# Performance work log

Measured on AMD Instinct MI355X. Metric: run time of the kernel, lower is better.

Reference implementation:

```python
import jax, jax.numpy as jnp
import numpy as np
from jax import lax

B, N, D, H, FF, K = 8192, 20, 128, 8, 512, 3  # batch*time, nodes, d_model, heads, ffn_dim, conv kernel
EPS = 1e-5


def _ln(x, w, b):
    m = jnp.mean(x, axis=-1, keepdims=True)
    v = jnp.mean((x - m) ** 2, axis=-1, keepdims=True)
    return (x - m) * lax.rsqrt(v + EPS) * w + b


def _conv1d(x, w):
    # x: (B,N,D) -> NCH layout (B,D,N); w: (D_out, D_in, K); SAME padding, no bias
    y = lax.conv_general_dilated(x.transpose(0, 2, 1), w, (1,), 'SAME',
                                 dimension_numbers=('NCH', 'OIH', 'NCH'))
    return y.transpose(0, 2, 1)  # back to (B,N,D)


def setup_inputs() -> dict:
    key = jax.random.key(0)
    ks = jax.random.split(key, 12)
    s = 0.05
    return {
        'x': jax.random.normal(ks[0], (B, N, D), jnp.float32),
        # conv1d QKV projection weights (out_ch, in_ch, kernel)
        'wq': jax.random.normal(ks[1], (D, D, K), jnp.float32) * s,
        'wk': jax.random.normal(ks[2], (D, D, K), jnp.float32) * s,
        'wv': jax.random.normal(ks[3], (D, D, K), jnp.float32) * s,
        # LayerNorms after each conv projection
        'lnq_w': jnp.ones((D,), jnp.float32), 'lnq_b': jnp.zeros((D,), jnp.float32),
        'lnk_w': jnp.ones((D,), jnp.float32), 'lnk_b': jnp.zeros((D,), jnp.float32),
        'lnv_w': jnp.ones((D,), jnp.float32), 'lnv_b': jnp.zeros((D,), jnp.float32),
        # relative position bias table (2N-1, H), trunc_normal std=0.02 approximated
        'rel_table': jax.random.normal(ks[4], (2 * N - 1, H), jnp.float32) * 0.02,
        # global spatial bias (H,N,N) and its learned scale alpha
        'gbias': jax.random.normal(ks[5], (H, N, N), jnp.float32) * 0.02,
        'alpha': jnp.array(1.0, jnp.float32),
        # attention output projection (stored as (in,out): y = x @ wo + bo)
        'wo': jax.random.normal(ks[6], (D, D), jnp.float32) * s,
        'bo': jnp.zeros((D,), jnp.float32),
        # FFN
        'w1': jax.random.normal(ks[7], (D, FF), jnp.float32) * s,
        'b1': jnp.zeros((FF,), jnp.float32),
        'w2': jax.random.normal(ks[8], (FF, D), jnp.float32) * s,
        'b2': jnp.zeros((D,), jnp.float32),
        # encoder LayerNorms
        'n1_w': jnp.ones((D,), jnp.float32), 'n1_b': jnp.zeros((D,), jnp.float32),
        'n2_w': jnp.ones((D,), jnp.float32), 'n2_b': jnp.zeros((D,), jnp.float32),
    }


def reference(x, wq, wk, wv, lnq_w, lnq_b, lnk_w, lnk_b, lnv_w, lnv_b,
              rel_table, gbias, alpha, wo, bo, w1, b1, w2, b2,
              n1_w, n1_b, n2_w, n2_b):
    b = x.shape[0]
    dk = D // H
    # conv QKV projections, each followed by LayerNorm + residual add (eval mode: dropout = identity)
    q = x + _ln(_conv1d(x, wq), lnq_w, lnq_b)
    k = x + _ln(_conv1d(x, wk), lnk_w, lnk_b)
    v = x + _ln(_conv1d(x, wv), lnv_w, lnv_b)
    qh = q.reshape(b, N, H, dk)
    kh = k.reshape(b, N, H, dk)
    vh = v.reshape(b, N, H, dk)
    scores = jnp.einsum('bnhd,bmhd->bhnm', qh, kh) * (1.0 / np.sqrt(dk))
    # relative position bias lookup: (N,N) index into (2N-1,H) table -> (H,N,N)
    idx = jnp.arange(N)[:, None] - jnp.arange(N)[None, :] + (N - 1)
    rpb = rel_table[idx].transpose(2, 0, 1)
    scores = scores + rpb[None] + gbias[None] * alpha
    attn = jax.nn.softmax(scores, axis=-1)
    ctx = jnp.einsum('bhnm,bmhd->bnhd', attn, vh).reshape(b, N, D)
    attn_out = ctx @ wo + bo
    # encoder: residual -> norm1 -> FFN -> residual -> norm2 (post-LN style)
    xr = _ln(x + attn_out, n1_w, n1_b)
    ffn = jax.nn.gelu(xr @ w1 + b1, approximate=False) @ w2 + b2
    return _ln(xr + ffn, n2_w, n2_b)
```

## Files before the change

### kernel.cpp

```cpp
#include <hip/hip_runtime.h>
#include <hip/hip_bf16.h>
#include <math.h>

#define NB 8192
#define NN 20
#define DD 128
#define HH 8
#define FFD 512
#define NROWS (NB * NN)

typedef __attribute__((ext_vector_type(8))) short bf16x8;
typedef __attribute__((ext_vector_type(4))) float f32x4;

__device__ __forceinline__ unsigned short f2bf(float f) {
  union { __hip_bfloat16 h; unsigned short u; } cv; cv.h = __float2bfloat16(f); return cv.u;
}
__device__ __forceinline__ float bf2f(unsigned short u) {
  union { unsigned short u; __hip_bfloat16 h; } cv; cv.u = u; return __bfloat162float(cv.h);
}
__device__ __forceinline__ float gelu_t(float v) {
  float t  = v * v;
  float u2 = v * fmaf(0.0713548162f, t, 1.5957691216f);
  float e  = __expf(u2);
  float r  = __builtin_amdgcn_rcpf(e + 1.0f);
  return fmaf(-v, r, v);
}
__device__ __forceinline__ void gload16(const unsigned short* g, unsigned short* lds) {
  __builtin_amdgcn_global_load_lds(
      (const __attribute__((address_space(1))) unsigned int*)g,
      (__attribute__((address_space(3))) unsigned int*)lds, 16, 0, 0);
}

__global__ __launch_bounds__(256) void prep2(
    const float* __restrict__ wq, const float* __restrict__ wk, const float* __restrict__ wv,
    const float* __restrict__ w1, const float* __restrict__ w2, const float* __restrict__ wo,
    const float* __restrict__ rel, const float* __restrict__ gb, const float* __restrict__ alpha,
    unsigned short* __restrict__ WcF, unsigned short* __restrict__ w1F,
    unsigned short* __restrict__ w2F, unsigned short* __restrict__ woF,
    float* __restrict__ biasT)
{
  int bid = blockIdx.x, t = threadIdx.x;
  if (bid < 288) {
    int nt = bid / 12, kc = bid % 12;
    for (int i = t; i < 512; i += 256) {
      int lane = i >> 3, j = i & 7;
      int k = kc * 32 + (lane >> 4) * 8 + j;
      int c = nt * 16 + (lane & 15);
      int kk = k >> 7, din = k & 127;
      int which = c >> 7, dout = c & 127;
      const float* w = (which == 0) ? wq : (which == 1) ? wk : wv;
      WcF[((nt * 12 + kc) * 64 + lane) * 8 + j] = f2bf(w[(dout * 128 + din) * 3 + kk]);
    }
  } else if (bid < 416) {
    int tt = bid - 288; int nt = tt / 4, kc = tt % 4;
    for (int i = t; i < 512; i += 256) {
      int lane = i >> 3, j = i & 7;
      int k = kc * 32 + (lane >> 4) * 8 + j;
      int c = nt * 16 + (lane & 15);
      w1F[((nt * 4 + kc) * 64 + lane) * 8 + j] = f2bf(w1[k * 512 + c]);
    }
  } else if (bid < 544) {
    int tt = bid - 416; int nt = tt / 16, kc = tt % 16;
    for (int i = t; i < 512; i += 256) {
      int lane = i >> 3, j = i & 7;
      int k = kc * 32 + (lane >> 4) * 8 + j;
      int c = nt * 16 + (lane & 15);
      w2F[((nt * 16 + kc) * 64 + lane) * 8 + j] = f2bf(w2[k * 128 + c]);
    }
  } else if (bid < 576) {
    int tt = bid - 544; int nt = tt / 4, kc = tt % 4;
    for (int i = t; i < 512; i += 256) {
      int lane = i >> 3, j = i & 7;
      int k = kc * 32 + (lane >> 4) * 8 + j;
      int c = nt * 16 + (lane & 15);
      woF[((nt * 4 + kc) * 64 + lane) * 8 + j] = f2bf(wo[k * 128 + c]);
    }
  } else {
    int h = bid - 576; float a = alpha[0];
    for (int i = t; i < 400; i += 256) {
      int n = i / 20, m = i % 20;
      biasT[h * 400 + i] = rel[(n - m + 19) * 8 + h] + gb[h * 400 + i] * a;
    }
  }
}

__global__ __launch_bounds__(256, 3) void conv_qkv(
    const float* __restrict__ x, const unsigned short* __restrict__ WcF,
    const float* __restrict__ lnq_w, const float* __restrict__ lnq_b,
    const float* __restrict__ lnk_w, const float* __restrict__ lnk_b,
    const float* __restrict__ lnv_w, const float* __restrict__ lnv_b,
    unsigned short* __restrict__ qP, unsigned short* __restrict__ kP,
    unsigned short* __restrict__ vP)
{
  __shared__ __align__(16) unsigned short xA[130 * 136];
  __shared__ __align__(16) unsigned short Bb[2][4096];
  unsigned short* Obuf = &Bb[0][0];

  const int t = threadIdx.x;
  const int w = t >> 6, l = t & 63;
  const int l15 = l & 15, l4 = l >> 4;
  const long g0 = (long)blockIdx.x * 128;
  const int chunkA = w * 2, chunkB = w * 2 + 1;

  gload16(WcF + (size_t)(chunkA * 12) * 512 + l * 8, &Bb[0][chunkA * 512]);
  gload16(WcF + (size_t)(chunkB * 12) * 512 + l * 8, &Bb[0][chunkB * 512]);

  for (int i = t; i < 130 * 32; i += 256) {
    int r = i >> 5, c4 = i & 31;
    long g = g0 - 1 + r;
    long gc = g < 0 ? 0 : (g >= NROWS ? NROWS - 1 : g);
    float4 v = *(const float4*)(x + gc * 128 + c4 * 4);
    ushort4 pk; pk.x = f2bf(v.x); pk.y = f2bf(v.y); pk.z = f2bf(v.z); pk.w = f2bf(v.w);
    *(ushort4*)&xA[r * 136 + c4 * 4] = pk;
  }
  __syncthreads();

  const int rA0 = w * 32 + l15;
  const int rA1 = rA0 + 16;
  const int nA0 = (int)((g0 + rA0) % 20);
  const int nA1 = (int)((g0 + rA1) % 20);
  bool mk0[3], mk1[3];
  mk0[0] = (nA0 != 0);  mk0[1] = true; mk0[2] = (nA0 != 19);
  mk1[0] = (nA1 != 0);  mk1[1] = true; mk1[2] = (nA1 != 19);

  const bf16x8 zz = {};
  for (int p = 0; p < 3; ++p) {
    const size_t Wpo = (size_t)p * 8 * 12 * 512;

    f32x4 acc[2][8];
    #pragma unroll
    for (int mt = 0; mt < 2; ++mt)
      #pragma unroll
      for (int nt = 0; nt < 8; ++nt) acc[mt][nt] = (f32x4){0.f, 0.f, 0.f, 0.f};

    for (int kc = 0; kc < 12; ++kc) {
      if (kc < 11) {
        int nb = (kc + 1) & 1;
        gload16(WcF + Wpo + (size_t)(chunkA * 12 + kc + 1) * 512 + l * 8, &Bb[nb][chunkA * 512]);
        gload16(WcF + Wpo + (size_t)(chunkB * 12 + kc + 1) * 512 + l * 8, &Bb[nb][chunkB * 512]);
      }
      const int kk = kc >> 2, k4 = kc & 3;
      bf16x8 a0 = *(const bf16x8*)&xA[(rA0 + kk) * 136 + k4 * 32 + l4 * 8]; if (!mk0[kk]) a0 = zz;
      bf16x8 a1 = *(const bf16x8*)&xA[(rA1 + kk) * 136 + k4 * 32 + l4 * 8]; if (!mk1[kk]) a1 = zz;
      const unsigned short* bb = &Bb[kc & 1][l * 8];
      #pragma unroll
      for (int nt = 0; nt < 8; ++nt) {
        bf16x8 b = *(const bf16x8*)(bb + nt * 512);
        acc[0][nt] = __builtin_amdgcn_mfma_f32_16x16x32_bf16(a0, b, acc[0][nt], 0, 0, 0);
        acc[1][nt] = __builtin_amdgcn_mfma_f32_16x16x32_bf16(a1, b, acc[1][nt], 0, 0, 0);
      }
      __syncthreads();
    }

    const float* lw = (p == 0) ? lnq_w : (p == 1) ? lnk_w : lnv_w;
    const float* lb = (p == 0) ? lnq_b : (p == 1) ? lnk_b : lnv_b;
    const float qs = (p == 0) ? 0.25f : 1.0f;
    unsigned short* plane = (p == 0) ? qP : (p == 1) ? kP : vP;
    float gw8[8], gb8[8];
    #pragma unroll
    for (int nt = 0; nt < 8; ++nt) { gw8[nt] = lw[nt * 16 + l15]; gb8[nt] = lb[nt * 16 + l15]; }

    float meanv[2][4], invv[2][4];
    #pragma unroll
    for (int mt = 0; mt < 2; ++mt) {
      float s[4], qq[4];
      #pragma unroll
      for (int j = 0; j < 4; ++j) {
        float a0 = 0.f, a1 = 0.f;
        #pragma unroll
        for (int nt = 0; nt < 8; ++nt) { float v = acc[mt][nt][j]; a0 += v; a1 = fmaf(v, v, a1); }
        s[j] = a0; qq[j] = a1;
      }
      #pragma unroll
      for (int off = 1; off < 16; off <<= 1) {
        #pragma unroll
        for (int j = 0; j < 4; ++j) { s[j] += __shfl_xor(s[j], off); qq[j] += __shfl_xor(qq[j], off); }
      }
      #pragma unroll
      for (int j = 0; j < 4; ++j) {
        float mean = s[j] * (1.f / 128.f);
        float var  = qq[j] * (1.f / 128.f) - mean * mean;
        meanv[mt][j] = mean;
        invv[mt][j]  = rsqrtf(var + 1e-5f);
      }
    }

    #pragma unroll
    for (int q = 0; q < 2; ++q) {
      #pragma unroll
      for (int mt = 0; mt < 2; ++mt)
        #pragma unroll
        for (int j = 0; j < 4; ++j) {
          int lr = w * 32 + mt * 16 + l4 * 4 + j;
          #pragma unroll
          for (int ntl = 0; ntl < 4; ++ntl) {
            int nt = q * 4 + ntl;
            Obuf[lr * 64 + ntl * 16 + l15] =
                f2bf((acc[mt][nt][j] - meanv[mt][j]) * invv[mt][j] * gw8[nt] + gb8[nt]);
          }
        }
      __syncthreads();
      #pragma unroll
      for (int it = 0; it < 4; ++it) {
        int i = t + it * 256;
        int r = i >> 3, c8 = i & 7;
        bf16x8 ob = *(const bf16x8*)&Obuf[r * 64 + c8 * 8];
        bf16x8 xr8 = *(const bf16x8*)&xA[(r + 1) * 136 + q * 64 + c8 * 8];
        bf16x8 o;
        #pragma unroll
        for (int j = 0; j < 8; ++j)
          o[j] = (short)f2bf((bf2f((unsigned short)xr8[j]) + bf2f((unsigned short)ob[j])) * qs);
        *(bf16x8*)&plane[(g0 + r) * 128 + q * 64 + c8 * 8] = o;
      }
      __syncthreads();
    }

    if (p < 2) {
      size_t Wn = (size_t)(p + 1) * 8 * 12 * 512;
      gload16(WcF + Wn + (size_t)(chunkA * 12) * 512 + l * 8, &Bb[0][chunkA * 512]);
      gload16(WcF + Wn + (size_t)(chunkB * 12) * 512 + l * 8, &Bb[0][chunkB * 512]);
      __syncthreads();
    }
  }
}

__global__ __launch_bounds__(256, 3) void attn_wo(
    const float* __restrict__ x,
    const unsigned short* __restrict__ qP, const unsigned short* __restrict__ kP,
    const unsigned short* __restrict__ vP,
    const unsigned short* __restrict__ woF, const float* __restrict__ biasT,
    const float* __restrict__ bo,
    const float* __restrict__ n1w, const float* __restrict__ n1b,
    unsigned short* __restrict__ xr)
{
  __shared__ __align__(16) char smem[43520];
  unsigned short* ks  = (unsigned short*)smem;
  unsigned short* vs  = (unsigned short*)(smem + 21760);
  unsigned short* ctx = ks;
  unsigned short* scr = vs;

  const int t = threadIdx.x;
  const int w = t >> 6, l = t & 63;
  const int l15 = l & 15, l4 = l >> 4;
  const int eb = blockIdx.x * 4;

  for (int i = t; i < 2560; i += 256) {
    int proj = i / 1280, r = i % 1280;
    int e = r / 320, rr = r % 320;
    int n = rr / 16, c8 = rr % 16;
    const unsigned short* src = (proj == 0 ? kP : vP) + (((size_t)(eb + e) * 20 + n) * 128 + c8 * 8);
    unsigned short* dst = (proj == 0 ? ks : vs) + ((e * 20 + n) * 136 + c8 * 8);
    *(bf16x8*)dst = *(const bf16x8*)src;
  }
  __syncthreads();

  float pm[3][20];
  #pragma unroll
  for (int pass = 0; pass < 3; ++pass) {
    int i = t + pass * 256;
    if (i < 640) {
      int e = i / 160, hh = (i / 20) % 8, n = i % 20;
      const unsigned short* qr = qP + ((size_t)(eb + e) * 20 + n) * 128 + hh * 16;
      bf16x8 qa = *(const bf16x8*)qr, qb = *(const bf16x8*)(qr + 8);
      float q[16];
      #pragma unroll
      for (int j = 0; j < 8; ++j) { q[j] = bf2f((unsigned short)qa[j]); q[8 + j] = bf2f((unsigned short)qb[j]); }
      float bias[20];
      const float* bp = &biasT[(hh * 20 + n) * 20];
      #pragma unroll
      for (int m4 = 0; m4 < 5; ++m4) {
        float4 bv = *(const float4*)(bp + m4 * 4);
        bias[m4 * 4] = bv.x; bias[m4 * 4 + 1] = bv.y; bias[m4 * 4 + 2] = bv.z; bias[m4 * 4 + 3] = bv.w;
      }
      float mx = -1e30f;
      #pragma unroll
      for (int m = 0; m < 20; ++m) {
        const unsigned short* kr = &ks[(e * 20 + m) * 136 + hh * 16];
        bf16x8 ka = *(const bf16x8*)kr, kb = *(const bf16x8*)(kr + 8);
        float sv = bias[m];
        #pragma unroll
        for (int j = 0; j < 8; ++j) {
          sv = fmaf(q[j], bf2f((unsigned short)ka[j]), sv);
          sv = fmaf(q[8 + j], bf2f((unsigned short)kb[j]), sv);
        }
        pm[pass][m] = sv; mx = fmaxf(mx, sv);
      }
      float sum = 0.f;
      #pragma unroll
      for (int m = 0; m < 20; ++m) { pm[pass][m] = __expf(pm[pass][m] - mx); sum += pm[pass][m]; }
      float rs = 1.f / sum;
      #pragma unroll
      for (int m = 0; m < 20; ++m) pm[pass][m] *= rs;
    }
  }
  __syncthreads();

  #pragma unroll
  for (int pass = 0; pass < 3; ++pass) {
    int i = t + pass * 256;
    if (i < 640) {
      int e = i / 160, hh = (i / 20) % 8, n = i % 20;
      float c[16];
      #pragma unroll
      for (int j = 0; j < 16; ++j) c[j] = 0.f;
      #pragma unroll
      for (int m = 0; m < 20; ++m) {
        const unsigned short* vr = &vs[(e * 20 + m) * 136 + hh * 16];
        bf16x8 va = *(const bf16x8*)vr, vb = *(const bf16x8*)(vr + 8);
        float pv = pm[pass][m];
        #pragma unroll
        for (int j = 0; j < 8; ++j) {
          c[j] = fmaf(pv, bf2f((unsigned short)va[j]), c[j]);
          c[8 + j] = fmaf(pv, bf2f((unsigned short)vb[j]), c[8 + j]);
        }
      }
      bf16x8 c0, c1;
      #pragma unroll
      for (int j = 0; j < 8; ++j) { c0[j] = (short)f2bf(c[j]); c1[j] = (short)f2bf(c[8 + j]); }
      *(bf16x8*)&ctx[(e * 20 + n) * 136 + hh * 16] = c0;
      *(bf16x8*)&ctx[(e * 20 + n) * 136 + hh * 16 + 8] = c1;
    }
  }
  __syncthreads();

  {
    f32x4 acc[5][2];
    #pragma unroll
    for (int mt = 0; mt < 5; ++mt)
      #pragma unroll
      for (int i = 0; i < 2; ++i) acc[mt][i] = (f32x4){0.f, 0.f, 0.f, 0.f};
    #pragma unroll
    for (int kc = 0; kc < 4; ++kc) {
      bf16x8 a[5], b[2];
      #pragma unroll
      for (int mt = 0; mt < 5; ++mt) {
        int g = mt * 16 + l15;
        int e = g / 20, n = g % 20;
        a[mt] = *(const bf16x8*)&ctx[(e * 20 + n) * 136 + kc * 32 + l4 * 8];
      }
      #pragma unroll
      for (int i = 0; i < 2; ++i) {
        int ntg = w * 2 + i;
        b[i] = *(const bf16x8*)&woF[((ntg * 4 + kc) * 64 + l) * 8];
      }
      #pragma unroll
      for (int mt = 0; mt < 5; ++mt)
        #pragma unroll
        for (int i = 0; i < 2; ++i)
          acc[mt][i] = __builtin_amdgcn_mfma_f32_16x16x32_bf16(a[mt], b[i], acc[mt][i], 0, 0, 0);
    }
    #pragma unroll
    for (int mt = 0; mt < 5; ++mt)
      #pragma unroll
      for (int i = 0; i < 2; ++i) {
        int col = (w * 2 + i) * 16 + l15;
        int gbase = mt * 16 + l4 * 4;
        #pragma unroll
        for (int j = 0; j < 4; ++j)
          scr[(gbase + j) * 136 + col] = f2bf(acc[mt][i][j]);
      }
  }
  __syncthreads();

  for (int r = w; r < 80; r += 4) {
    int e = r / 20, n = r % 20;
    const float* xrow = x + ((size_t)(eb + e) * 20 + n) * 128;
    float v0 = bf2f(scr[r * 136 + l])      + bo[l]      + xrow[l];
    float v1 = bf2f(scr[r * 136 + 64 + l]) + bo[64 + l] + xrow[64 + l];
    float s = v0 + v1, sq = v0 * v0 + v1 * v1;
    #pragma unroll
    for (int off = 32; off > 0; off >>= 1) { s += __shfl_xor(s, off); sq += __shfl_xor(sq, off); }
    float mean = s * (1.f / 128.f);
    float var  = sq * (1.f / 128.f) - mean * mean;
    float inv  = rsqrtf(var + 1e-5f);
    size_t ro = ((size_t)(eb + e) * 20 + n) * 128;
    xr[ro + l]      = f2bf((v0 - mean) * inv * n1w[l] + n1b[l]);
    xr[ro + 64 + l] = f2bf((v1 - mean) * inv * n1w[64 + l] + n1b[64 + l]);
  }
}

__global__ __launch_bounds__(256, 4) void ffn_c(
    const unsigned short* __restrict__ xr,
    const unsigned short* __restrict__ w1F, const unsigned short* __restrict__ w2F,
    const float* __restrict__ b1, const float* __restrict__ b2,
    const float* __restrict__ n2w, const float* __restrict__ n2b,
    float* __restrict__ out)
{
  __shared__ __align__(16) unsigned short smem[2 * 64 * 136];
  unsigned short* xrb = smem;
  unsigned short* hq  = smem + 64 * 136;
  unsigned short* scr = hq;

  const int t = threadIdx.x;
  const int w = t >> 6, l = t & 63;
  const int l15 = l & 15, l4 = l >> 4;
  const size_t row0 = (size_t)blockIdx.x * 64;

  for (int i = t; i < 1024; i += 256) {
    int r = i >> 4, c8 = i & 15;
    *(bf16x8*)&xrb[r * 136 + c8 * 8] = *(const bf16x8*)&xr[(row0 + r) * 128 + c8 * 8];
  }
  __syncthreads();

  f32x4 acc2[4][2];
  #pragma unroll
  for (int mt = 0; mt < 4; ++mt)
    #pragma unroll
    for (int i = 0; i < 2; ++i) acc2[mt][i] = (f32x4){0.f, 0.f, 0.f, 0.f};

  #pragma unroll
  for (int ph = 0; ph < 4; ++ph) {
    f32x4 acc1[4][2];
    #pragma unroll
    for (int mt = 0; mt < 4; ++mt)
      #pragma unroll
      for (int i = 0; i < 2; ++i) acc1[mt][i] = (f32x4){0.f, 0.f, 0.f, 0.f};
    #pragma unroll
    for (int kc = 0; kc < 4; ++kc) {
      bf16x8 a[4];
      #pragma unroll
      for (int mt = 0; mt < 4; ++mt)
        a[mt] = *(const bf16x8*)&xrb[(mt * 16 + l15) * 136 + kc * 32 + l4 * 8];
      #pragma unroll
      for (int i = 0; i < 2; ++i) {
        int ntg = ph * 8 + w * 2 + i;
        bf16x8 b = *(const bf16x8*)&w1F[((ntg * 4 + kc) * 64 + l) * 8];
        #pragma unroll
        for (int mt = 0; mt < 4; ++mt)
          acc1[mt][i] = __builtin_amdgcn_mfma_f32_16x16x32_bf16(a[mt], b, acc1[mt][i], 0, 0, 0);
      }
    }
    #pragma unroll
    for (int i = 0; i < 2; ++i) {
      int lc = (w * 2 + i) * 16 + l15;
      float b1v = b1[(ph * 8 + w * 2 + i) * 16 + l15];
      #pragma unroll
      for (int mt = 0; mt < 4; ++mt)
        #pragma unroll
        for (int j = 0; j < 4; ++j) {
          float v = acc1[mt][i][j] + b1v;
          hq[(mt * 16 + l4 * 4 + j) * 136 + lc] = f2bf(gelu_t(v));
        }
    }
    __syncthreads();

    #pragma unroll
    for (int kk = 0; kk < 4; ++kk) {
      bf16x8 a[4];
      #pragma unroll
      for (int mt = 0; mt < 4; ++mt)
        a[mt] = *(const bf16x8*)&hq[(mt * 16 + l15) * 136 + kk * 32 + l4 * 8];
      #pragma unroll
      for (int i = 0; i < 2; ++i) {
        int ntg = w * 2 + i;
        int kcg = ph * 4 + kk;
        bf16x8 b = *(const bf16x8*)&w2F[((ntg * 16 + kcg) * 64 + l) * 8];
        #pragma unroll
        for (int mt = 0; mt < 4; ++mt)
          acc2[mt][i] = __builtin_amdgcn_mfma_f32_16x16x32_bf16(a[mt], b, acc2[mt][i], 0, 0, 0);
      }
    }
    __syncthreads();
  }

  #pragma unroll
  for (int mt = 0; mt < 4; ++mt)
    #pragma unroll
    for (int i = 0; i < 2; ++i) {
      int col = (w * 2 + i) * 16 + l15;
      int rbase = mt * 16 + l4 * 4;
      #pragma unroll
      for (int j = 0; j < 4; ++j)
        scr[(rbase + j) * 136 + col] = f2bf(acc2[mt][i][j]);
    }
  __syncthreads();

  for (int r = w; r < 64; r += 4) {
    float v0 = bf2f(scr[r * 136 + l])      + b2[l]      + bf2f(xrb[r * 136 + l]);
    float v1 = bf2f(scr[r * 136 + 64 + l]) + b2[64 + l] + bf2f(xrb[r * 136 + 64 + l]);
    float s = v0 + v1, sq = v0 * v0 + v1 * v1;
    #pragma unroll
    for (int off = 32; off > 0; off >>= 1) { s += __shfl_xor(s, off); sq += __shfl_xor(sq, off); }
    float mean = s * (1.f / 128.f);
    float var  = sq * (1.f / 128.f) - mean * mean;
    float inv  = rsqrtf(var + 1e-5f);
    out[(row0 + r) * 128 + l]      = (v0 - mean) * inv * n2w[l] + n2b[l];
    out[(row0 + r) * 128 + 64 + l] = (v1 - mean) * inv * n2w[64 + l] + n2b[64 + l];
  }
}

extern "C" void kernel_launch(void* const* d_in, const int* in_sizes, int n_in,
                              void* d_out, int out_size, void* d_ws, size_t ws_size,
                              hipStream_t stream) {
  const float* x     = (const float*)d_in[0];
  const float* wq    = (const float*)d_in[1];
  const float* wk    = (const float*)d_in[2];
  const float* wv    = (const float*)d_in[3];
  const float* lnq_w = (const float*)d_in[4];
  const float* lnq_b = (const float*)d_in[5];
  const float* lnk_w = (const float*)d_in[6];
  const float* lnk_b = (const float*)d_in[7];
  const float* lnv_w = (const float*)d_in[8];
  const float* lnv_b = (const float*)d_in[9];
  const float* rel   = (const float*)d_in[10];
  const float* gb    = (const float*)d_in[11];
  const float* alpha = (const float*)d_in[12];
  const float* wo    = (const float*)d_in[13];
  const float* bo    = (const float*)d_in[14];
  const float* w1    = (const float*)d_in[15];
  const float* b1    = (const float*)d_in[16];
  const float* w2    = (const float*)d_in[17];
  const float* b2    = (const float*)d_in[18];
  const float* n1w   = (const float*)d_in[19];
  const float* n1b   = (const float*)d_in[20];
  const float* n2w   = (const float*)d_in[21];
  const float* n2b   = (const float*)d_in[22];
  float* out = (float*)d_out;

  unsigned short* WcF = (unsigned short*)d_ws;
  unsigned short* w1F = WcF + 147456;
  unsigned short* w2F = w1F + 65536;
  unsigned short* woF = w2F + 65536;
  float* biasT = (float*)(woF + 16384);
  unsigned short* xr = (unsigned short*)((char*)d_ws + 602624);

  const size_t NEED2 = 602624ULL + 41943040ULL;

  hipLaunchKernelGGL(prep2, dim3(584), dim3(256), 0, stream,
                     wq, wk, wv, w1, w2, wo, rel, gb, alpha, WcF, w1F, w2F, woF, biasT);

  unsigned short* qP = (unsigned short*)((char*)d_ws + NEED2);
  unsigned short* kP = (unsigned short*)d_out;
  unsigned short* vP = kP + (size_t)NROWS * 128;

  hipLaunchKernelGGL(conv_qkv, dim3(NROWS / 128), dim3(256), 0, stream,
                     x, WcF, lnq_w, lnq_b, lnk_w, lnk_b, lnv_w, lnv_b, qP, kP, vP);
  hipLaunchKernelGGL(attn_wo, dim3(NB / 4), dim3(256), 0, stream,
                     x, qP, kP, vP, woF, biasT, bo, n1w, n1b, xr);
  hipLaunchKernelGGL(ffn_c, dim3(NROWS / 64), dim3(256), 0, stream,
                     xr, w1F, w2F, b1, b2, n2w, n2b, out);
}
```

Before: 276.6 us.

## Swizzle attention LDS layout to drop padding and raise occupancy to four blocks

Replaces the 136-element padded LDS row stride in attn_wo with an unpadded 128 stride plus an XOR swizzle for the ctx and scratch tiles. This shrinks shared memory from 43520 to 40960 bytes and raises the launch bound from 3 to 4 blocks per CU. The QK dot product is also split into four independent accumulators to shorten the FMA dependency chain. K and V reads are left unswizzled at stride 128, which risks LDS bank conflicts, and the tighter register budget may cause spills.

```diff
diff --git a/kernel.cpp b/kernel.cpp
--- a/kernel.cpp
+++ b/kernel.cpp
@@ -29,6 +29,9 @@
   __builtin_amdgcn_global_load_lds(
       (const __attribute__((address_space(1))) unsigned int*)g,
       (__attribute__((address_space(3))) unsigned int*)lds, 16, 0, 0);
+}
+__device__ __forceinline__ int swz80(int row, int col) {
+  return row * 128 + ((((col >> 3) ^ (row & 15)) << 3) | (col & 7));
 }
 
 __global__ __launch_bounds__(256) void prep2(
@@ -224,7 +227,7 @@
   }
 }
 
-__global__ __launch_bounds__(256, 3) void attn_wo(
+__global__ __launch_bounds__(256, 4) void attn_wo(
     const float* __restrict__ x,
     const unsigned short* __restrict__ qP, const unsigned short* __restrict__ kP,
     const unsigned short* __restrict__ vP,
@@ -233,9 +236,9 @@
     const float* __restrict__ n1w, const float* __restrict__ n1b,
     unsigned short* __restrict__ xr)
 {
-  __shared__ __align__(16) char smem[43520];
+  __shared__ __align__(16) char smem[40960];
   unsigned short* ks  = (unsigned short*)smem;
-  unsigned short* vs  = (unsigned short*)(smem + 21760);
+  unsigned short* vs  = (unsigned short*)(smem + 20480);
   unsigned short* ctx = ks;
   unsigned short* scr = vs;
 
@@ -249,7 +252,7 @@
     int e = r / 320, rr = r % 320;
     int n = rr / 16, c8 = rr % 16;
     const unsigned short* src = (proj == 0 ? kP : vP) + (((size_t)(eb + e) * 20 + n) * 128 + c8 * 8);
-    unsigned short* dst = (proj == 0 ? ks : vs) + ((e * 20 + n) * 136 + c8 * 8);
+    unsigned short* dst = (proj == 0 ? ks : vs) + ((e * 20 + n) * 128 + c8 * 8);
     *(bf16x8*)dst = *(const bf16x8*)src;
   }
   __syncthreads();
@@ -275,14 +278,17 @@
       float mx = -1e30f;
       #pragma unroll
       for (int m = 0; m < 20; ++m) {
-        const unsigned short* kr = &ks[(e * 20 + m) * 136 + hh * 16];
+        const unsigned short* kr = &ks[(e * 20 + m) * 128 + hh * 16];
         bf16x8 ka = *(const bf16x8*)kr, kb = *(const bf16x8*)(kr + 8);
-        float sv = bias[m];
-        #pragma unroll
-        for (int j = 0; j < 8; ++j) {
-          sv = fmaf(q[j], bf2f((unsigned short)ka[j]), sv);
-          sv = fmaf(q[8 + j], bf2f((unsigned short)kb[j]), sv);
+        float s0 = bias[m], s1 = 0.f, s2 = 0.f, s3 = 0.f;
+        #pragma unroll
+        for (int j = 0; j < 4; ++j) {
+          s0 = fmaf(q[j],      bf2f((unsigned short)ka[j]),     s0);
+          s1 = fmaf(q[j + 4],  bf2f((unsigned short)ka[j + 4]), s1);
+          s2 = fmaf(q[j + 8],  bf2f((unsigned short)kb[j]),     s2);
+          s3 = fmaf(q[j + 12], bf2f((unsigned short)kb[j + 4]), s3);
         }
+        float sv = (s0 + s1) + (s2 + s3);
         pm[pass][m] = sv; mx = fmaxf(mx, sv);
       }
       float sum = 0.f;
@@ -305,7 +311,7 @@
       for (int j = 0; j < 16; ++j) c[j] = 0.f;
       #pragma unroll
       for (int m = 0; m < 20; ++m) {
-        const unsigned short* vr = &vs[(e * 20 + m) * 136 + hh * 16];
+        const unsigned short* vr = &vs[(e * 20 + m) * 128 + hh * 16];
         bf16x8 va = *(const bf16x8*)vr, vb = *(const bf16x8*)(vr + 8);
         float pv = pm[pass][m];
         #pragma unroll
@@ -317,8 +323,9 @@
       bf16x8 c0, c1;
       #pragma unroll
       for (int j = 0; j < 8; ++j) { c0[j] = (short)f2bf(c[j]); c1[j] = (short)f2bf(c[8 + j]); }
-      *(bf16x8*)&ctx[(e * 20 + n) * 136 + hh * 16] = c0;
-      *(bf16x8*)&ctx[(e * 20 + n) * 136 + hh * 16 + 8] = c1;
+      int re = e * 20 + n;
+      *(bf16x8*)&ctx[swz80(re, hh * 16)]     = c0;
+      *(bf16x8*)&ctx[swz80(re, hh * 16 + 8)] = c1;
     }
   }
   __syncthreads();
@@ -333,11 +340,8 @@
     for (int kc = 0; kc < 4; ++kc) {
       bf16x8 a[5], b[2];
       #pragma unroll
-      for (int mt = 0; mt < 5; ++mt) {
-        int g = mt * 16 + l15;
-        int e = g / 20, n = g % 20;
-        a[mt] = *(const bf16x8*)&ctx[(e * 20 + n) * 136 + kc * 32 + l4 * 8];
-      }
+      for (int mt = 0; mt < 5; ++mt)
+        a[mt] = *(const bf16x8*)&ctx[swz80(mt * 16 + l15, kc * 32 + l4 * 8)];
       #pragma unroll
       for (int i = 0; i < 2; ++i) {
         int ntg = w * 2 + i;
@@ -354,10 +358,10 @@
       #pragma unroll
       for (int i = 0; i < 2; ++i) {
         int col = (w * 2 + i) * 16 + l15;
-        int gbase = mt * 16 + l4 * 4;
+        int rbase = mt * 16 + l4 * 4;
         #pragma unroll
         for (int j = 0; j < 4; ++j)
-          scr[(gbase + j) * 136 + col] = f2bf(acc[mt][i][j]);
+          scr[swz80(rbase + j, col)] = f2bf(acc[mt][i][j]);
       }
   }
   __syncthreads();
@@ -365,8 +369,8 @@
   for (int r = w; r < 80; r += 4) {
     int e = r / 20, n = r % 20;
     const float* xrow = x + ((size_t)(eb + e) * 20 + n) * 128;
-    float v0 = bf2f(scr[r * 136 + l])      + bo[l]      + xrow[l];
-    float v1 = bf2f(scr[r * 136 + 64 + l]) + bo[64 + l] + xrow[64 + l];
+    float v0 = bf2f(scr[swz80(r, l)])      + bo[l]      + xrow[l];
+    float v1 = bf2f(scr[swz80(r, l + 64)]) + bo[64 + l] + xrow[64 + l];
     float s = v0 + v1, sq = v0 * v0 + v1 * v1;
     #pragma unroll
     for (int off = 32; off > 0; off >>= 1) { s += __shfl_xor(s, off); sq += __shfl_xor(sq, off); }
```

Result: slower. 325.1 us (+17.5%).

## Store Q/K/V and context in fp16 and use packed dot2 for attention

Applied to the files above, without the earlier changes.

Switches the Q/K/V planes, context buffer, Wo weights and output scratch from bf16 to fp16. The score computation uses packed fp16 dot2 instructions with fp32 accumulation, and the P·V accumulation uses packed half2 multiply-adds. This removes the per-element bf16-to-fp32 conversions and halves the ALU work in the per-thread attention loops, and the Wo projection moves to the fp16 MFMA. In exchange it risks overflow or precision loss, because the P·V sum now accumulates in fp16 and the activations are stored in a narrower-range format.

```diff
diff --git a/kernel.cpp b/kernel.cpp
--- a/kernel.cpp
+++ b/kernel.cpp
@@ -11,12 +11,29 @@
 
 typedef __attribute__((ext_vector_type(8))) short bf16x8;
 typedef __attribute__((ext_vector_type(4))) float f32x4;
+typedef __attribute__((ext_vector_type(2))) _Float16 h2;
+typedef __attribute__((ext_vector_type(8))) _Float16 f16x8;
+
+#if defined(__has_builtin)
+#if __has_builtin(__builtin_amdgcn_fdot2)
+#define FDOT2(a, b, c) __builtin_amdgcn_fdot2((a), (b), (c), false)
+#endif
+#endif
+#ifndef FDOT2
+#define FDOT2(a, b, c) (fmaf((float)(a).x, (float)(b).x, fmaf((float)(a).y, (float)(b).y, (c))))
+#endif
 
 __device__ __forceinline__ unsigned short f2bf(float f) {
   union { __hip_bfloat16 h; unsigned short u; } cv; cv.h = __float2bfloat16(f); return cv.u;
 }
 __device__ __forceinline__ float bf2f(unsigned short u) {
   union { unsigned short u; __hip_bfloat16 h; } cv; cv.u = u; return __bfloat162float(cv.h);
+}
+__device__ __forceinline__ unsigned short f2h_bits(float f) {
+  union { _Float16 h; unsigned short u; } cv; cv.h = (_Float16)f; return cv.u;
+}
+__device__ __forceinline__ float h2f_bits(unsigned short u) {
+  union { unsigned short u; _Float16 h; } cv; cv.u = u; return (float)cv.h;
 }
 __device__ __forceinline__ float gelu_t(float v) {
   float t  = v * v;
@@ -73,7 +90,7 @@
       int lane = i >> 3, j = i & 7;
       int k = kc * 32 + (lane >> 4) * 8 + j;
       int c = nt * 16 + (lane & 15);
-      woF[((nt * 4 + kc) * 64 + lane) * 8 + j] = f2bf(wo[k * 128 + c]);
+      woF[((nt * 4 + kc) * 64 + lane) * 8 + j] = f2h_bits(wo[k * 128 + c]);
     }
   } else {
     int h = bid - 576; float a = alpha[0];
@@ -206,11 +223,11 @@
         int r = i >> 3, c8 = i & 7;
         bf16x8 ob = *(const bf16x8*)&Obuf[r * 64 + c8 * 8];
         bf16x8 xr8 = *(const bf16x8*)&xA[(r + 1) * 136 + q * 64 + c8 * 8];
-        bf16x8 o;
+        unsigned short o[8];
         #pragma unroll
         for (int j = 0; j < 8; ++j)
-          o[j] = (short)f2bf((bf2f((unsigned short)xr8[j]) + bf2f((unsigned short)ob[j])) * qs);
-        *(bf16x8*)&plane[(g0 + r) * 128 + q * 64 + c8 * 8] = o;
+          o[j] = f2h_bits((bf2f((unsigned short)xr8[j]) + bf2f((unsigned short)ob[j])) * qs);
+        *(bf16x8*)&plane[(g0 + r) * 128 + q * 64 + c8 * 8] = *(const bf16x8*)o;
       }
       __syncthreads();
     }
@@ -261,10 +278,14 @@
     if (i < 640) {
       int e = i / 160, hh = (i / 20) % 8, n = i % 20;
       const unsigned short* qr = qP + ((size_t)(eb + e) * 20 + n) * 128 + hh * 16;
-      bf16x8 qa = *(const bf16x8*)qr, qb = *(const bf16x8*)(qr + 8);
-      float q[16];
-      #pragma unroll
-      for (int j = 0; j < 8; ++j) { q[j] = bf2f((unsigned short)qa[j]); q[8 + j] = bf2f((unsigned short)qb[j]); }
+      f16x8 qa = *(const f16x8*)qr;
+      f16x8 qb = *(const f16x8*)(qr + 8);
+      h2 qp[8];
+      #pragma unroll
+      for (int j = 0; j < 4; ++j) {
+        qp[j]     = (h2){qa[2 * j], qa[2 * j + 1]};
+        qp[4 + j] = (h2){qb[2 * j], qb[2 * j + 1]};
+      }
       float bias[20];
       const float* bp = &biasT[(hh * 20 + n) * 20];
       #pragma unroll
@@ -276,13 +297,17 @@
       #pragma unroll
       for (int m = 0; m < 20; ++m) {
         const unsigned short* kr = &ks[(e * 20 + m) * 136 + hh * 16];
-        bf16x8 ka = *(const bf16x8*)kr, kb = *(const bf16x8*)(kr + 8);
-        float sv = bias[m];
-        #pragma unroll
-        for (int j = 0; j < 8; ++j) {
-          sv = fmaf(q[j], bf2f((unsigned short)ka[j]), sv);
-          sv = fmaf(q[8 + j], bf2f((unsigned short)kb[j]), sv);
-        }
+        f16x8 ka = *(const f16x8*)kr;
+        f16x8 kb = *(const f16x8*)(kr + 8);
+        float s0 = FDOT2(qp[0], ((h2){ka[0], ka[1]}), bias[m]);
+        float s1 = FDOT2(qp[1], ((h2){ka[2], ka[3]}), 0.f);
+        float s2 = FDOT2(qp[2], ((h2){ka[4], ka[5]}), 0.f);
+        float s3 = FDOT2(qp[3], ((h2){ka[6], ka[7]}), 0.f);
+        s0 = FDOT2(qp[4], ((h2){kb[0], kb[1]}), s0);
+        s1 = FDOT2(qp[5], ((h2){kb[2], kb[3]}), s1);
+        s2 = FDOT2(qp[6], ((h2){kb[4], kb[5]}), s2);
+        s3 = FDOT2(qp[7], ((h2){kb[6], kb[7]}), s3);
+        float sv = (s0 + s1) + (s2 + s3);
         pm[pass][m] = sv; mx = fmaxf(mx, sv);
       }
       float sum = 0.f;
@@ -300,25 +325,31 @@
     int i = t + pass * 256;
     if (i < 640) {
       int e = i / 160, hh = (i / 20) % 8, n = i % 20;
-      float c[16];
-      #pragma unroll
-      for (int j = 0; j < 16; ++j) c[j] = 0.f;
+      h2 c2[8];
+      #pragma unroll
+      for (int j = 0; j < 8; ++j) c2[j] = (h2){(_Float16)0.f, (_Float16)0.f};
       #pragma unroll
       for (int m = 0; m < 20; ++m) {
         const unsigned short* vr = &vs[(e * 20 + m) * 136 + hh * 16];
-        bf16x8 va = *(const bf16x8*)vr, vb = *(const bf16x8*)(vr + 8);
-        float pv = pm[pass][m];
-        #pragma unroll
-        for (int j = 0; j < 8; ++j) {
-          c[j] = fmaf(pv, bf2f((unsigned short)va[j]), c[j]);
-          c[8 + j] = fmaf(pv, bf2f((unsigned short)vb[j]), c[8 + j]);
+        f16x8 va = *(const f16x8*)vr;
+        f16x8 vb = *(const f16x8*)(vr + 8);
+        _Float16 ph = (_Float16)pm[pass][m];
+        h2 pp = (h2){ph, ph};
+        #pragma unroll
+        for (int j = 0; j < 4; ++j) {
+          c2[j]     += pp * (h2){va[2 * j], va[2 * j + 1]};
+          c2[4 + j] += pp * (h2){vb[2 * j], vb[2 * j + 1]};
         }
       }
-      bf16x8 c0, c1;
-      #pragma unroll
-      for (int j = 0; j < 8; ++j) { c0[j] = (short)f2bf(c[j]); c1[j] = (short)f2bf(c[8 + j]); }
-      *(bf16x8*)&ctx[(e * 20 + n) * 136 + hh * 16] = c0;
-      *(bf16x8*)&ctx[(e * 20 + n) * 136 + hh * 16 + 8] = c1;
+      f16x8 o0, o1;
+      #pragma unroll
+      for (int j = 0; j < 4; ++j) {
+        o0[2 * j] = c2[j].x;     o0[2 * j + 1] = c2[j].y;
+        o1[2 * j] = c2[4 + j].x; o1[2 * j + 1] = c2[4 + j].y;
+      }
+      unsigned short* cw = &ctx[(e * 20 + n) * 136 + hh * 16];
+      *(f16x8*)cw = o0;
+      *(f16x8*)(cw + 8) = o1;
     }
   }
   __syncthreads();
@@ -331,23 +362,22 @@
       for (int i = 0; i < 2; ++i) acc[mt][i] = (f32x4){0.f, 0.f, 0.f, 0.f};
     #pragma unroll
     for (int kc = 0; kc < 4; ++kc) {
-      bf16x8 a[5], b[2];
+      f16x8 a[5], b[2];
       #pragma unroll
       for (int mt = 0; mt < 5; ++mt) {
         int g = mt * 16 + l15;
-        int e = g / 20, n = g % 20;
-        a[mt] = *(const bf16x8*)&ctx[(e * 20 + n) * 136 + kc * 32 + l4 * 8];
+        a[mt] = *(const f16x8*)&ctx[g * 136 + kc * 32 + l4 * 8];
       }
       #pragma unroll
       for (int i = 0; i < 2; ++i) {
         int ntg = w * 2 + i;
-        b[i] = *(const bf16x8*)&woF[((ntg * 4 + kc) * 64 + l) * 8];
+        b[i] = *(const f16x8*)&woF[((ntg * 4 + kc) * 64 + l) * 8];
       }
       #pragma unroll
       for (int mt = 0; mt < 5; ++mt)
         #pragma unroll
         for (int i = 0; i < 2; ++i)
-          acc[mt][i] = __builtin_amdgcn_mfma_f32_16x16x32_bf16(a[mt], b[i], acc[mt][i], 0, 0, 0);
+          acc[mt][i] = __builtin_amdgcn_mfma_f32_16x16x32_f16(a[mt], b[i], acc[mt][i], 0, 0, 0);
     }
     #pragma unroll
     for (int mt = 0; mt < 5; ++mt)
@@ -357,7 +387,7 @@
         int gbase = mt * 16 + l4 * 4;
         #pragma unroll
         for (int j = 0; j < 4; ++j)
-          scr[(gbase + j) * 136 + col] = f2bf(acc[mt][i][j]);
+          scr[(gbase + j) * 136 + col] = f2h_bits(acc[mt][i][j]);
       }
   }
   __syncthreads();
@@ -365,8 +395,8 @@
   for (int r = w; r < 80; r += 4) {
     int e = r / 20, n = r % 20;
     const float* xrow = x + ((size_t)(eb + e) * 20 + n) * 128;
-    float v0 = bf2f(scr[r * 136 + l])      + bo[l]      + xrow[l];
-    float v1 = bf2f(scr[r * 136 + 64 + l]) + bo[64 + l] + xrow[64 + l];
+    float v0 = h2f_bits(scr[r * 136 + l])      + bo[l]      + xrow[l];
+    float v1 = h2f_bits(scr[r * 136 + 64 + l]) + bo[64 + l] + xrow[64 + l];
     float s = v0 + v1, sq = v0 * v0 + v1 * v1;
     #pragma unroll
     for (int off = 32; off > 0; off >>= 1) { s += __shfl_xor(s, off); sq += __shfl_xor(sq, off); }
```

New measurement: 269.4 us. 2.6% less time.
